# Kernel optimization log

Measured on AMD Instinct MI355X. Metric: run time of the kernel, lower is better.

Reference implementation:

```python
import jax, jax.numpy as jnp
import numpy as np

D_MODEL = 768
N_HEAD = 12
D_FF = 3072
EPS = 1e-5


def _layer_norm(x, w, b):
    mu = jnp.mean(x, axis=-1, keepdims=True)
    var = jnp.mean(jnp.square(x - mu), axis=-1, keepdims=True)
    return (x - mu) * jax.lax.rsqrt(var + EPS) * w + b


def setup_inputs() -> dict:
    key = jax.random.key(0)
    ks = jax.random.split(key, 8)
    B, S, D = 2, 4096, D_MODEL
    s_in = 1.0 / np.sqrt(D)
    s_ff = 1.0 / np.sqrt(D_FF)
    return {
        "src": jax.random.normal(ks[0], (B, S, D), jnp.float32),
        "w_qkv": jax.random.uniform(ks[1], (3 * D, D), jnp.float32, -s_in, s_in),
        "b_qkv": jnp.zeros((3 * D,), jnp.float32),
        "w_out": jax.random.uniform(ks[2], (D, D), jnp.float32, -s_in, s_in),
        "b_out": jnp.zeros((D,), jnp.float32),
        "w1": jax.random.uniform(ks[3], (D_FF, D), jnp.float32, -s_in, s_in),
        "b1": jnp.zeros((D_FF,), jnp.float32),
        "w2": jax.random.uniform(ks[4], (D, D_FF), jnp.float32, -s_ff, s_ff),
        "b2": jnp.zeros((D,), jnp.float32),
        "ln1_w": jnp.ones((D,), jnp.float32),
        "ln1_b": jnp.zeros((D,), jnp.float32),
        "ln2_w": jnp.ones((D,), jnp.float32),
        "ln2_b": jnp.zeros((D,), jnp.float32),
    }


def reference(src, w_qkv, b_qkv, w_out, b_out, w1, b1, w2, b2,
              ln1_w, ln1_b, ln2_w, ln2_b):
    B, S, D = src.shape
    H, dh = N_HEAD, D // N_HEAD
    # fused QKV projection: [B,S,3D]
    qkv = jnp.einsum('bsd,ed->bse', src, w_qkv) + b_qkv
    q, k, v = jnp.split(qkv, 3, axis=-1)
    q = q.reshape(B, S, H, dh)
    k = k.reshape(B, S, H, dh)
    v = v.reshape(B, S, H, dh)
    scale = 1.0 / np.sqrt(dh)
    scores = jnp.einsum('bqhd,bkhd->bhqk', q, k) * scale  # [B,H,S,S]
    attn = jax.nn.softmax(scores, axis=-1)
    ctx = jnp.einsum('bhqk,bkhd->bqhd', attn, v).reshape(B, S, D)
    attn_out = jnp.einsum('bsd,ed->bse', ctx, w_out) + b_out
    # post-norm residual (norm_first=False), dropout inactive in eval
    x = _layer_norm(src + attn_out, ln1_w, ln1_b)
    h = jax.nn.relu(jnp.einsum('bsd,fd->bsf', x, w1) + b1)
    ffn = jnp.einsum('bsf,df->bsd', h, w2) + b2
    return _layer_norm(x + ffn, ln2_w, ln2_b)
```

## Files before the change

### kernel.cpp

```cpp
#include <hip/hip_runtime.h>
#include <hip/hip_bf16.h>

typedef __hip_bfloat16 bf16;
typedef __attribute__((ext_vector_type(8))) short s16x8;
typedef __attribute__((ext_vector_type(4))) float f32x4;

#define MFMA16x16x32(A, B, C) __builtin_amdgcn_mfma_f32_16x16x32_bf16((A), (B), (C), 0, 0, 0)

__device__ __forceinline__ void async_copy16(const bf16* g, bf16* l) {
  __builtin_amdgcn_global_load_lds(
      (const __attribute__((address_space(1))) void*)g,
      (__attribute__((address_space(3))) void*)l, 16, 0, 0);
}

__device__ __forceinline__ int SW(int row, int chunk) {
  return row * 64 + (((chunk) ^ (row & 7)) << 3);
}

__global__ __launch_bounds__(256)
void cast_all_kernel(const float* __restrict__ s0, bf16* __restrict__ d0,
                     const float* __restrict__ s1, bf16* __restrict__ d1,
                     const float* __restrict__ s2, bf16* __restrict__ d2,
                     const float* __restrict__ s3, bf16* __restrict__ d3,
                     const float* __restrict__ s4, bf16* __restrict__ d4) {
  int blk = blockIdx.x;
  const float* in; bf16* out;
  if (blk < 1728)      { in = s0; out = d0; }
  else if (blk < 2304) { in = s1; out = d1; blk -= 1728; }
  else if (blk < 4608) { in = s2; out = d2; blk -= 2304; }
  else if (blk < 6912) { in = s3; out = d3; blk -= 4608; }
  else                 { in = s4; out = d4; blk -= 6912; }
  const int i = (blk * 256 + threadIdx.x) * 4;
  const float4 f = *(const float4*)(in + i);
  out[i + 0] = (bf16)f.x; out[i + 1] = (bf16)f.y;
  out[i + 2] = (bf16)f.z; out[i + 3] = (bf16)f.w;
}

template <int RELU, int VT, int ACCUM, typename OutT>
__global__ __launch_bounds__(256)
void gemm_bt_kernel(const bf16* __restrict__ A, const bf16* __restrict__ B,
                    const float* __restrict__ bias, OutT* __restrict__ C,
                    int N, int K, int lda, int ldb, bf16* __restrict__ C2) {
  __shared__ __align__(16) bf16 As[2][128 * 32];
  __shared__ __align__(16) bf16 Bs[2][128 * 32];

  const int t = threadIdx.x;
  const int lane = t & 63;
  const int wave = t >> 6;
  const int wm = (wave >> 1) << 6;
  const int wn = (wave & 1) << 6;
  const int col16 = lane & 15;
  const int quad = lane >> 4;
  const int bm = blockIdx.x;
  const int bn = blockIdx.y;
  const int kz = (VT == 3) ? blockIdx.z * K : 0;

  const bf16* Ag = A + (size_t)(bm * 128 + (t >> 2)) * lda + (t & 3) * 8 + kz;
  const bf16* Bg = B + (size_t)(bn * 128 + (t >> 2)) * ldb + (t & 3) * 8 + kz;

  f32x4 acc[4][4] = {};

  async_copy16(Ag, &As[0][0] + t * 8);
  async_copy16(Ag + (size_t)64 * lda, &As[0][0] + 2048 + t * 8);
  async_copy16(Bg, &Bs[0][0] + t * 8);
  async_copy16(Bg + (size_t)64 * ldb, &Bs[0][0] + 2048 + t * 8);

  int n = 0;
  for (int k0 = 0; k0 < K; k0 += 32, n ^= 1) {
    __syncthreads();
    if (k0 + 32 < K) {
      const int k1 = k0 + 32;
      async_copy16(Ag + k1, &As[n ^ 1][0] + t * 8);
      async_copy16(Ag + (size_t)64 * lda + k1, &As[n ^ 1][0] + 2048 + t * 8);
      async_copy16(Bg + k1, &Bs[n ^ 1][0] + t * 8);
      async_copy16(Bg + (size_t)64 * ldb + k1, &Bs[n ^ 1][0] + 2048 + t * 8);
    }
    const bf16* asn = &As[n][0];
    const bf16* bsn = &Bs[n][0];

    s16x8 af[4], bfr[4];
#pragma unroll
    for (int i = 0; i < 4; i++)
      af[i] = *(const s16x8*)(asn + (wm + i * 16 + col16) * 32 + quad * 8);
#pragma unroll
    for (int j = 0; j < 4; j++)
      bfr[j] = *(const s16x8*)(bsn + (wn + j * 16 + col16) * 32 + quad * 8);
#pragma unroll
    for (int i = 0; i < 4; i++)
#pragma unroll
      for (int j = 0; j < 4; j++)
        acc[i][j] = MFMA16x16x32(af[i], bfr[j], acc[i][j]);
  }

  const int row0 = bm * 128 + wm + quad * 4;
  const int col0 = bn * 128 + wn + col16;
#pragma unroll
  for (int j = 0; j < 4; j++) {
    const int col = col0 + j * 16;
    const float bv = (ACCUM || (VT == 3 && blockIdx.z)) ? 0.0f : bias[col];
#pragma unroll
    for (int i = 0; i < 4; i++) {
#pragma unroll
      for (int r = 0; r < 4; r++) {
        float v = acc[i][j][r] + bv;
        if (RELU) v = fmaxf(v, 0.0f);
        const int row = row0 + i * 16 + r;
        if (VT == 2) {
          if (col < 1536) {
            C[(size_t)row * N + col] = (OutT)v;
          } else {
            const int cc = col - 1536;
            C2[(size_t)((row >> 12) * 12 + (cc >> 6)) * 262144 +
               (cc & 63) * 4096 + (row & 4095)] = (bf16)v;
          }
        } else if (VT == 3) {
          ((float*)(blockIdx.z ? (void*)C2 : (void*)C))[(size_t)row * N + col] = v;
        } else {
          const size_t idx = (size_t)row * N + col;
          if (ACCUM) v += ((const float*)C)[idx];
          C[idx] = (OutT)v;
        }
      }
    }
  }
}

__global__ __launch_bounds__(256, 2)
void attn_kernel(const bf16* __restrict__ QK, const bf16* __restrict__ Vt,
                 bf16* __restrict__ Opart, float* __restrict__ lbuf) {
  __shared__ __align__(16) bf16 Ks[2][64 * 64];
  __shared__ __align__(16) bf16 Vs[2][64 * 64];
  __shared__ __align__(16) bf16 Ps[4][64 * 64];

  const int t = threadIdx.x, lane = t & 63, wave = t >> 6;
  const int col16 = lane & 15, quad = lane >> 4;
  const int b = blockIdx.z, h = blockIdx.y;
  const int ks = blockIdx.x >> 4;
  const int qblk = blockIdx.x & 15;
  const int qw0 = qblk * 256 + wave * 64;

  s16x8 bq[4][2];
#pragma unroll
  for (int qt = 0; qt < 4; qt++)
#pragma unroll
    for (int s = 0; s < 2; s++) {
      union { s16x8 v; bf16 hh[8]; } u;
      u.v = *(const s16x8*)(QK + (size_t)(b * 4096 + qw0 + qt * 16 + col16) * 1536 +
                            h * 64 + s * 32 + quad * 8);
#pragma unroll
      for (int e = 0; e < 8; e++) u.hh[e] = (bf16)((float)u.hh[e] * 0.18033688f);
      bq[qt][s] = u.v;
    }

  union { s16x8 v; short s_[8]; } uo1;
#pragma unroll
  for (int e = 0; e < 8; e++) uo1.s_[e] = (short)0x3F80;
  const s16x8 aones = uo1.v;

  const int srow = t >> 3;
  const int schx = (t & 7) ^ (srow & 7);
  const bf16* kgb = QK + (size_t)(b * 4096) * 1536 + 768 + h * 64;
  const bf16* vgb = Vt + (size_t)(b * 12 + h) * 262144;
  const bf16* ksrc0 = kgb + (size_t)srow * 1536 + schx * 8;
  const bf16* ksrc1 = kgb + (size_t)(32 + srow) * 1536 + schx * 8;
  const bf16* vsrc0 = vgb + (size_t)srow * 4096 + schx * 8;
  const bf16* vsrc1 = vgb + (size_t)(32 + srow) * 4096 + schx * 8;

  f32x4 o[4][4] = {};
  f32x4 lacc[4] = {};
  bf16* pw = &Ps[wave][0];

  const int kbeg = ks * 2048, kend = kbeg + 2048;

  async_copy16(ksrc0 + (size_t)kbeg * 1536, &Ks[0][0] + t * 8);
  async_copy16(ksrc1 + (size_t)kbeg * 1536, &Ks[0][0] + 2048 + t * 8);
  async_copy16(vsrc0 + kbeg, &Vs[0][0] + t * 8);
  async_copy16(vsrc1 + kbeg, &Vs[0][0] + 2048 + t * 8);

  int n = 0;
  for (int k0 = kbeg; k0 < kend; k0 += 64, n ^= 1) {
    __syncthreads();
    if (k0 + 64 < kend) {
      const int k1 = k0 + 64;
      async_copy16(ksrc0 + (size_t)k1 * 1536, &Ks[n ^ 1][0] + t * 8);
      async_copy16(ksrc1 + (size_t)k1 * 1536, &Ks[n ^ 1][0] + 2048 + t * 8);
      async_copy16(vsrc0 + k1, &Vs[n ^ 1][0] + t * 8);
      async_copy16(vsrc1 + k1, &Vs[n ^ 1][0] + 2048 + t * 8);
    }
    const bf16* ksn = &Ks[n][0];
    const bf16* vsn = &Vs[n][0];

    s16x8 ak[2][4];
#pragma unroll
    for (int s = 0; s < 2; s++)
#pragma unroll
      for (int kt = 0; kt < 4; kt++)
        ak[s][kt] = *(const s16x8*)(ksn + SW(kt * 16 + col16, s * 4 + quad));

#pragma unroll
    for (int kt = 0; kt < 4; kt++) {
      f32x4 st[4] = {};
#pragma unroll
      for (int s = 0; s < 2; s++)
#pragma unroll
        for (int qt = 0; qt < 4; qt++)
          st[qt] = MFMA16x16x32(ak[s][kt], bq[qt][s], st[qt]);
#pragma unroll
      for (int qt = 0; qt < 4; qt++) {
        union { unsigned long long u; bf16 hh[4]; } pk;
#pragma unroll
        for (int r = 0; r < 4; r++)
          pk.hh[r] = (bf16)__builtin_amdgcn_exp2f(st[qt][r]);
        *(unsigned long long*)(pw + (qt * 16 + col16) * 64 +
                               (((kt * 2 + (quad >> 1)) ^ (col16 & 7)) << 3) +
                               (quad & 1) * 4) = pk.u;
      }
    }
    asm volatile("s_waitcnt lgkmcnt(0)" ::: "memory");

#pragma unroll
    for (int s = 0; s < 2; s++) {
      s16x8 bp[4];
#pragma unroll
      for (int qt = 0; qt < 4; qt++)
        bp[qt] = *(const s16x8*)(pw + SW(qt * 16 + col16, s * 4 + quad));
#pragma unroll
      for (int qt = 0; qt < 4; qt++)
        lacc[qt] = MFMA16x16x32(aones, bp[qt], lacc[qt]);
#pragma unroll
      for (int dt = 0; dt < 4; dt++) {
        const s16x8 av = *(const s16x8*)(vsn + SW(dt * 16 + col16, s * 4 + quad));
#pragma unroll
        for (int qt = 0; qt < 4; qt++)
          o[dt][qt] = MFMA16x16x32(av, bp[qt], o[dt][qt]);
      }
    }
  }

  if (lane < 16) {
#pragma unroll
    for (int qt = 0; qt < 4; qt++)
      lbuf[(size_t)ks * 98304 + (size_t)(b * 4096 + qw0 + qt * 16 + lane) * 12 + h] =
          lacc[qt][0];
  }

#pragma unroll
  for (int qt = 0; qt < 4; qt++)
#pragma unroll
    for (int dt = 0; dt < 4; dt++)
#pragma unroll
      for (int r = 0; r < 4; r++)
        pw[(qt * 16 + col16) * 64 + (((dt * 2 + (quad >> 1)) ^ (col16 & 7)) << 3) +
           (quad & 1) * 4 + r] = (bf16)(o[dt][qt][r]);
  asm volatile("s_waitcnt lgkmcnt(0)" ::: "memory");
  const int qrow = lane >> 1, chalf = (lane & 1) * 4;
#pragma unroll
  for (int h2 = 0; h2 < 2; h2++) {
    const int rl = h2 * 32 + qrow;
    bf16* dst = Opart + (size_t)ks * 6291456 +
                (size_t)(b * 4096 + qw0 + rl) * 768 + h * 64 + chalf * 8;
#pragma unroll
    for (int i = 0; i < 4; i++)
      *(s16x8*)(dst + i * 8) = *(const s16x8*)(pw + SW(rl, chalf + i));
  }
}

__global__ __launch_bounds__(256)
void attn_combine_kernel(const bf16* __restrict__ Opart,
                         const float* __restrict__ lbuf,
                         bf16* __restrict__ ctx) {
  const int i = blockIdx.x * 256 + threadIdx.x;
  const int row = i / 96, c8 = i % 96;
  const int h = c8 >> 3;
  const float inv = 1.0f / (lbuf[(size_t)row * 12 + h] +
                            lbuf[98304 + (size_t)row * 12 + h]);
  union { s16x8 v; bf16 hh[8]; } ua, ub, uo;
  ua.v = *(const s16x8*)(Opart + (size_t)row * 768 + c8 * 8);
  ub.v = *(const s16x8*)(Opart + 6291456 + (size_t)row * 768 + c8 * 8);
#pragma unroll
  for (int j = 0; j < 8; j++)
    uo.hh[j] = (bf16)(((float)ua.hh[j] + (float)ub.hh[j]) * inv);
  *(s16x8*)(ctx + (size_t)row * 768 + c8 * 8) = uo.v;
}

__global__ __launch_bounds__(256)
void add_ln_b_kernel(const float* __restrict__ X, const float* __restrict__ Y,
                     const float* __restrict__ Y2,
                     const float* __restrict__ w, const float* __restrict__ b,
                     bf16* __restrict__ out) {
  const int row = blockIdx.x * 4 + (threadIdx.x >> 6);
  const int lane = threadIdx.x & 63;
  const float* x = X + (size_t)row * 768;
  const float* y = Y + (size_t)row * 768;
  const float* y2 = Y2 + (size_t)row * 768;
  float v[12];
  float s = 0.0f;
#pragma unroll
  for (int i = 0; i < 3; i++) {
    const int c = lane * 4 + i * 256;
    const float4 xf = *(const float4*)(x + c);
    const float4 yf = *(const float4*)(y + c);
    const float4 zf = *(const float4*)(y2 + c);
    v[i * 4 + 0] = xf.x + yf.x + zf.x; v[i * 4 + 1] = xf.y + yf.y + zf.y;
    v[i * 4 + 2] = xf.z + yf.z + zf.z; v[i * 4 + 3] = xf.w + yf.w + zf.w;
    s += v[i * 4] + v[i * 4 + 1] + v[i * 4 + 2] + v[i * 4 + 3];
  }
#pragma unroll
  for (int off = 32; off > 0; off >>= 1) s += __shfl_xor(s, off, 64);
  const float mu = s * (1.0f / 768.0f);
  float var = 0.0f;
#pragma unroll
  for (int i = 0; i < 12; i++) { const float d = v[i] - mu; var += d * d; }
#pragma unroll
  for (int off = 32; off > 0; off >>= 1) var += __shfl_xor(var, off, 64);
  const float rs = rsqrtf(var * (1.0f / 768.0f) + 1e-5f);
#pragma unroll
  for (int i = 0; i < 12; i++) {
    const int c = lane * 4 + (i >> 2) * 256 + (i & 3);
    out[(size_t)row * 768 + c] = (bf16)((v[i] - mu) * rs * w[c] + b[c]);
  }
}

__global__ __launch_bounds__(256)
void add_ln_f_kernel(const bf16* __restrict__ X, const float* __restrict__ Y,
                     const float* __restrict__ w, const float* __restrict__ b,
                     float* __restrict__ out) {
  const int row = blockIdx.x * 4 + (threadIdx.x >> 6);
  const int lane = threadIdx.x & 63;
  const bf16* x = X + (size_t)row * 768;
  const float* y = Y + (size_t)row * 768;
  float v[12];
  float s = 0.0f;
#pragma unroll
  for (int i = 0; i < 3; i++) {
    const int c = lane * 4 + i * 256;
    const float4 yf = *(const float4*)(y + c);
    v[i * 4 + 0] = (float)x[c + 0] + yf.x; v[i * 4 + 1] = (float)x[c + 1] + yf.y;
    v[i * 4 + 2] = (float)x[c + 2] + yf.z; v[i * 4 + 3] = (float)x[c + 3] + yf.w;
    s += v[i * 4] + v[i * 4 + 1] + v[i * 4 + 2] + v[i * 4 + 3];
  }
#pragma unroll
  for (int off = 32; off > 0; off >>= 1) s += __shfl_xor(s, off, 64);
  const float mu = s * (1.0f / 768.0f);
  float var = 0.0f;
#pragma unroll
  for (int i = 0; i < 12; i++) { const float d = v[i] - mu; var += d * d; }
#pragma unroll
  for (int off = 32; off > 0; off >>= 1) var += __shfl_xor(var, off, 64);
  const float rs = rsqrtf(var * (1.0f / 768.0f) + 1e-5f);
#pragma unroll
  for (int i = 0; i < 12; i++) {
    const int c = lane * 4 + (i >> 2) * 256 + (i & 3);
    out[(size_t)row * 768 + c] = (v[i] - mu) * rs * w[c] + b[c];
  }
}

extern "C" void kernel_launch(void* const* d_in, const int* in_sizes, int n_in,
                              void* d_out, int out_size, void* d_ws, size_t ws_size,
                              hipStream_t stream) {
  (void)in_sizes; (void)n_in; (void)out_size; (void)ws_size;
  const float* src   = (const float*)d_in[0];
  const float* w_qkv = (const float*)d_in[1];
  const float* b_qkv = (const float*)d_in[2];
  const float* w_out = (const float*)d_in[3];
  const float* b_out = (const float*)d_in[4];
  const float* w1    = (const float*)d_in[5];
  const float* b1    = (const float*)d_in[6];
  const float* w2    = (const float*)d_in[7];
  const float* b2    = (const float*)d_in[8];
  const float* ln1w  = (const float*)d_in[9];
  const float* ln1b  = (const float*)d_in[10];
  const float* ln2w  = (const float*)d_in[11];
  const float* ln2b  = (const float*)d_in[12];
  float* out = (float*)d_out;

  char* ws = (char*)d_ws;
  bf16* wqkvb = (bf16*)ws;
  bf16* woutb = (bf16*)(ws + 3538944);
  bf16* w1b   = (bf16*)(ws + 4718592);
  bf16* w2b   = (bf16*)(ws + 9437184);
  bf16* srcb  = (bf16*)(ws + 14155776);
  bf16* QK    = (bf16*)(ws + 26738688);
  bf16* Vt    = (bf16*)(ws + 51904512);
  bf16* Opart = (bf16*)d_out;
  float* lbuf = (float*)ws;
  bf16* ctx   = (bf16*)(ws + 14155776);
  float* woP0 = (float*)(ws + 26738688);
  float* woP1 = (float*)d_out;
  bf16* x1b   = (bf16*)(ws + 51904512);
  bf16* hbuf  = (bf16*)(ws + 14155776);
  float* ffn  = out;

  cast_all_kernel<<<13056, 256, 0, stream>>>(
      w_qkv, wqkvb, w_out, woutb, w1, w1b, w2, w2b, src, srcb);

  gemm_bt_kernel<0, 2, 0, bf16><<<dim3(64, 18), 256, 0, stream>>>(
      srcb, wqkvb, b_qkv, QK, 1536, 768, 768, 768, Vt);
  attn_kernel<<<dim3(32, 12, 2), 256, 0, stream>>>(QK, Vt, Opart, lbuf);
  attn_combine_kernel<<<3072, 256, 0, stream>>>(Opart, lbuf, ctx);
  gemm_bt_kernel<0, 3, 0, float><<<dim3(64, 6, 2), 256, 0, stream>>>(
      ctx, woutb, b_out, woP0, 768, 384, 768, 768, (bf16*)woP1);
  add_ln_b_kernel<<<2048, 256, 0, stream>>>(src, woP0, woP1, ln1w, ln1b, x1b);
  for (int c = 0; c < 2; c++) {
    gemm_bt_kernel<1, 0, 0, bf16><<<dim3(64, 12), 256, 0, stream>>>(
        x1b, w1b + (size_t)c * 1536 * 768, b1 + c * 1536, hbuf, 1536, 768, 768,
        768, nullptr);
    if (c == 0)
      gemm_bt_kernel<0, 0, 0, float><<<dim3(64, 6), 256, 0, stream>>>(
          hbuf, w2b + c * 1536, b2, ffn, 768, 1536, 1536, 3072, nullptr);
    else
      gemm_bt_kernel<0, 0, 1, float><<<dim3(64, 6), 256, 0, stream>>>(
          hbuf, w2b + c * 1536, b2, ffn, 768, 1536, 1536, 3072, nullptr);
  }
  add_ln_f_kernel<<<2048, 256, 0, stream>>>(x1b, ffn, ln2w, ln2b, out);
}
```

Measured before the change: 478.8 us.

## Halve attention P staging buffer by processing query tiles in two halves

Restructures the attention inner loop so that each wave computes scores, exponentiates and does the PV MFMAs for two 16-row query tiles at a time rather than all four. This halves the per-wave P shared-memory buffer, which lowers LDS use and may allow more resident blocks. V fragments are now loaded into registers once per key block and reused across both halves. The output epilogue is likewise split into two halves. The cost is more registers for V fragments and extra LDS wait points.

```diff
diff --git a/kernel.cpp b/kernel.cpp
--- a/kernel.cpp
+++ b/kernel.cpp
@@ -130,7 +130,7 @@
                  bf16* __restrict__ Opart, float* __restrict__ lbuf) {
   __shared__ __align__(16) bf16 Ks[2][64 * 64];
   __shared__ __align__(16) bf16 Vs[2][64 * 64];
-  __shared__ __align__(16) bf16 Ps[4][64 * 64];
+  __shared__ __align__(16) bf16 Ps[4][32 * 64];
 
   const int t = threadIdx.x, lane = t & 63, wave = t >> 6;
   const int col16 = lane & 15, quad = lane >> 4;
@@ -190,50 +190,61 @@
     const bf16* ksn = &Ks[n][0];
     const bf16* vsn = &Vs[n][0];
 
-    s16x8 ak[2][4];
+    s16x8 ak[2][4], av[2][4];
 #pragma unroll
     for (int s = 0; s < 2; s++)
 #pragma unroll
       for (int kt = 0; kt < 4; kt++)
         ak[s][kt] = *(const s16x8*)(ksn + SW(kt * 16 + col16, s * 4 + quad));
-
-#pragma unroll
-    for (int kt = 0; kt < 4; kt++) {
-      f32x4 st[4] = {};
+#pragma unroll
+    for (int s = 0; s < 2; s++)
+#pragma unroll
+      for (int dt = 0; dt < 4; dt++)
+        av[s][dt] = *(const s16x8*)(vsn + SW(dt * 16 + col16, s * 4 + quad));
+
+#pragma unroll
+    for (int hf = 0; hf < 2; hf++) {
+      f32x4 st[4][2] = {};
 #pragma unroll
       for (int s = 0; s < 2; s++)
 #pragma unroll
-        for (int qt = 0; qt < 4; qt++)
-          st[qt] = MFMA16x16x32(ak[s][kt], bq[qt][s], st[qt]);
-#pragma unroll
-      for (int qt = 0; qt < 4; qt++) {
-        union { unsigned long long u; bf16 hh[4]; } pk;
-#pragma unroll
-        for (int r = 0; r < 4; r++)
-          pk.hh[r] = (bf16)__builtin_amdgcn_exp2f(st[qt][r]);
-        *(unsigned long long*)(pw + (qt * 16 + col16) * 64 +
-                               (((kt * 2 + (quad >> 1)) ^ (col16 & 7)) << 3) +
-                               (quad & 1) * 4) = pk.u;
+        for (int kt = 0; kt < 4; kt++)
+#pragma unroll
+          for (int qh = 0; qh < 2; qh++)
+            st[kt][qh] = MFMA16x16x32(ak[s][kt], bq[2 * hf + qh][s], st[kt][qh]);
+
+#pragma unroll
+      for (int qh = 0; qh < 2; qh++) {
+#pragma unroll
+        for (int kt = 0; kt < 4; kt++) {
+          union { unsigned long long u; bf16 hh[4]; } pk;
+#pragma unroll
+          for (int r = 0; r < 4; r++)
+            pk.hh[r] = (bf16)__builtin_amdgcn_exp2f(st[kt][qh][r]);
+          *(unsigned long long*)(pw + (qh * 16 + col16) * 64 +
+                                 (((kt * 2 + (quad >> 1)) ^ (col16 & 7)) << 3) +
+                                 (quad & 1) * 4) = pk.u;
+        }
       }
-    }
-    asm volatile("s_waitcnt lgkmcnt(0)" ::: "memory");
-
-#pragma unroll
-    for (int s = 0; s < 2; s++) {
-      s16x8 bp[4];
-#pragma unroll
-      for (int qt = 0; qt < 4; qt++)
-        bp[qt] = *(const s16x8*)(pw + SW(qt * 16 + col16, s * 4 + quad));
-#pragma unroll
-      for (int qt = 0; qt < 4; qt++)
-        lacc[qt] = MFMA16x16x32(aones, bp[qt], lacc[qt]);
-#pragma unroll
-      for (int dt = 0; dt < 4; dt++) {
-        const s16x8 av = *(const s16x8*)(vsn + SW(dt * 16 + col16, s * 4 + quad));
-#pragma unroll
-        for (int qt = 0; qt < 4; qt++)
-          o[dt][qt] = MFMA16x16x32(av, bp[qt], o[dt][qt]);
+      asm volatile("s_waitcnt lgkmcnt(0)" ::: "memory");
+
+#pragma unroll
+      for (int s = 0; s < 2; s++) {
+        s16x8 bp[2];
+#pragma unroll
+        for (int qh = 0; qh < 2; qh++)
+          bp[qh] = *(const s16x8*)(pw + SW(qh * 16 + col16, s * 4 + quad));
+#pragma unroll
+        for (int qh = 0; qh < 2; qh++)
+          lacc[2 * hf + qh] = MFMA16x16x32(aones, bp[qh], lacc[2 * hf + qh]);
+#pragma unroll
+        for (int dt = 0; dt < 4; dt++)
+#pragma unroll
+          for (int qh = 0; qh < 2; qh++)
+            o[dt][2 * hf + qh] = MFMA16x16x32(av[s][dt], bp[qh], o[dt][2 * hf + qh]);
       }
+      if (hf == 0)
+        asm volatile("s_waitcnt lgkmcnt(0)" ::: "memory");
     }
   }
 
@@ -244,24 +255,26 @@
           lacc[qt][0];
   }
 
-#pragma unroll
-  for (int qt = 0; qt < 4; qt++)
-#pragma unroll
-    for (int dt = 0; dt < 4; dt++)
-#pragma unroll
-      for (int r = 0; r < 4; r++)
-        pw[(qt * 16 + col16) * 64 + (((dt * 2 + (quad >> 1)) ^ (col16 & 7)) << 3) +
-           (quad & 1) * 4 + r] = (bf16)(o[dt][qt][r]);
-  asm volatile("s_waitcnt lgkmcnt(0)" ::: "memory");
   const int qrow = lane >> 1, chalf = (lane & 1) * 4;
 #pragma unroll
-  for (int h2 = 0; h2 < 2; h2++) {
-    const int rl = h2 * 32 + qrow;
+  for (int hf = 0; hf < 2; hf++) {
+    if (hf)
+      asm volatile("s_waitcnt lgkmcnt(0)" ::: "memory");
+#pragma unroll
+    for (int qh = 0; qh < 2; qh++)
+#pragma unroll
+      for (int dt = 0; dt < 4; dt++)
+#pragma unroll
+        for (int r = 0; r < 4; r++)
+          pw[(qh * 16 + col16) * 64 +
+             (((dt * 2 + (quad >> 1)) ^ (col16 & 7)) << 3) +
+             (quad & 1) * 4 + r] = (bf16)(o[dt][2 * hf + qh][r]);
+    asm volatile("s_waitcnt lgkmcnt(0)" ::: "memory");
     bf16* dst = Opart + (size_t)ks * 6291456 +
-                (size_t)(b * 4096 + qw0 + rl) * 768 + h * 64 + chalf * 8;
+                (size_t)(b * 4096 + qw0 + hf * 32 + qrow) * 768 + h * 64 + chalf * 8;
 #pragma unroll
     for (int i = 0; i < 4; i++)
-      *(s16x8*)(dst + i * 8) = *(const s16x8*)(pw + SW(rl, chalf + i));
+      *(s16x8*)(dst + i * 8) = *(const s16x8*)(pw + SW(qrow, chalf + i));
   }
 }
 
```

New measurement: 487.6 us. No clear change (+1.8%).
